# Kernel optimization log

Measured on AMD Instinct MI355X. Metric: run time of the kernel, lower is better.

Reference implementation:

```python
import jax, jax.numpy as jnp
import numpy as np

N, L, E, H = 8, 1024, 512, 4


def setup_inputs() -> dict:
    key = jax.random.key(0)
    ks = jax.random.split(key, 10)
    s = 1.0 / np.sqrt(E)
    return {
        "modalA": jax.random.normal(ks[0], (N, L, E), dtype=jnp.float32),
        "modalB": jax.random.normal(ks[1], (N, L, E), dtype=jnp.float32),
        "WqA": jax.random.normal(ks[2], (E, E), dtype=jnp.float32) * s,
        "bqA": jax.random.normal(ks[3], (E,), dtype=jnp.float32) * s,
        "WkA": jax.random.normal(ks[4], (E, E), dtype=jnp.float32) * s,
        "bkA": jax.random.normal(ks[5], (E,), dtype=jnp.float32) * s,
        "WqB": jax.random.normal(ks[6], (E, E), dtype=jnp.float32) * s,
        "bqB": jax.random.normal(ks[7], (E,), dtype=jnp.float32) * s,
        "WkB": jax.random.normal(ks[8], (E, E), dtype=jnp.float32) * s,
        "bkB": jax.random.normal(ks[9], (E,), dtype=jnp.float32) * s,
    }


def reference(modalA, modalB, WqA, bqA, WkA, bkA, WqB, bqB, WkB, bkB):
    # torch Linear: y = x @ W.T + b
    qA = modalA @ WqA.T + bqA  # [N, L, E]
    kA = modalA @ WkA.T + bkA
    qB = modalB @ WqB.T + bqB
    kB = modalB @ WkB.T + bkB

    # mean over heads of per-head dot products == full-dim dot / num_heads
    # (algebraically identical to einsum('nqhd,nkhd->nhqk').mean(1))
    inv_scale = 1.0 / (H * np.sqrt(E).astype(np.float32))

    def attn(q, k):
        scores = jnp.einsum('nqd,nkd->nqk', q, k) * inv_scale  # [N, L, L]
        return jax.nn.softmax(scores, axis=-1)

    weighted_A = attn(qA, kA)
    weighted_B = attn(qB, kB)
    weighted_AB = attn(qA, kB)
    weighted_BA = attn(qB, kA)

    cat_lower = jnp.concatenate([weighted_A, weighted_AB], axis=-1)  # [N, L, 2L]
    cat_upper = jnp.concatenate([weighted_B, weighted_BA], axis=-1)  # [N, L, 2L]
    cat = jnp.concatenate([cat_lower, cat_upper], axis=1)            # [N, 2L, 2L]
    return jnp.mean(cat, axis=0)                                     # [2L, 2L]
```

## Files before the change

kernel.cpp:

```cpp
#include <hip/hip_runtime.h>
#include <hip/hip_bf16.h>

typedef __bf16 bf16;
typedef bf16 bf16x8 __attribute__((ext_vector_type(8)));
typedef _Float16 f16;
typedef f16 f16x8 __attribute__((ext_vector_type(8)));
typedef float f32x4 __attribute__((ext_vector_type(4)));

constexpr int LL = 1024;
constexpr int EE = 512;
constexpr int NBATCH = 8;

__device__ __forceinline__ f32x4 mfma16(bf16x8 a, bf16x8 b, f32x4 c) {
    return __builtin_amdgcn_mfma_f32_16x16x32_bf16(a, b, c, 0, 0, 0);
}

#define GLOAD_LDS16(g, l)                                                     \
    __builtin_amdgcn_global_load_lds(                                         \
        (const __attribute__((address_space(1))) void*)(g),                   \
        (__attribute__((address_space(3))) void*)(l), 16, 0, 0)

__device__ __forceinline__ void wave_barrier() {
    __asm__ volatile("" ::: "memory");
    __builtin_amdgcn_s_barrier();
    __asm__ volatile("" ::: "memory");
}

constexpr int WAIT_VM6 = 0xF76;
constexpr int WAIT_VM0 = 0xF70;

struct CvtParams {
    const float* src[4];
    bf16* dst[4];
    int n8[4];
};

__global__ __launch_bounds__(256) void cvt_kernel(CvtParams p) {
    const int y = blockIdx.y;
    const float* __restrict__ src = p.src[y];
    bf16* __restrict__ dst = p.dst[y];
    const int n8 = p.n8[y];
    for (int i = blockIdx.x * 256 + threadIdx.x; i < n8; i += gridDim.x * 256) {
        float4 a = *(const float4*)(src + (size_t)i * 8);
        float4 b = *(const float4*)(src + (size_t)i * 8 + 4);
        bf16x8 o;
        o[0] = (bf16)a.x; o[1] = (bf16)a.y; o[2] = (bf16)a.z; o[3] = (bf16)a.w;
        o[4] = (bf16)b.x; o[5] = (bf16)b.y; o[6] = (bf16)b.z; o[7] = (bf16)b.w;
        *(bf16x8*)(dst + (size_t)i * 8) = o;
    }
}

struct ProjParams {
    const float* x[4];
    const bf16* w[4];
    const float* b[4];
};

__global__ __launch_bounds__(256, 2) void proj_kernel(ProjParams p, bf16* __restrict__ outbase) {
    const int f = blockIdx.x;
    const int xcd = f & 7;
    const int u = f >> 3;
    const int mz = xcd >> 2;
    const int by = (xcd & 3) * 16 + (u & 15);
    const int zq = (u >> 4) & 1;
    const int bxp = u >> 5;
    const int z = mz * 2 + zq;

    const float* __restrict__ X = p.x[z];
    const bf16* __restrict__ W = p.w[z];
    const float* __restrict__ Bv = p.b[z];
    bf16* __restrict__ O = outbase + (size_t)z * (NBATCH * LL) * EE;

    __shared__ union {
        struct {
            alignas(16) float Af[2][128][32];
            alignas(16) bf16  Bs[2][256][32];
        } st;
        alignas(16) bf16 ep[64][264];
    } sm;

    const int t = threadIdx.x;
    const int lane = t & 63, wid = t >> 6;
    const int wm = wid & 1, wn = wid >> 1;
    const int lr = lane & 15, kg = lane >> 4;

    f32x4 acc[4][8] = {};

    const int ar = t >> 3;
    const int ac = t & 7;
    const int sA = (ar >> 1) & 7;
    const int agc = (ac ^ sA) * 4;
    const float* Xrow0 = X + (size_t)(by * 128 + ar) * EE + agc;

    const int srow = t >> 2;
    const int cgl = t & 3;
    const int gcg = (cgl ^ ((srow >> 1) & 3)) * 8;
    const int scg = (kg ^ ((lr >> 1) & 3)) * 8;
    const bf16* Wrow0 = W + (size_t)(bxp * 256 + srow) * EE + gcg;

    const int cgLo = (2 * kg) ^ ((lr >> 1) & 7);
    const int cgHi = cgLo ^ 1;

    auto stage = [&](int k, int b) {
        const int k0 = k * 32;
#pragma unroll
        for (int i = 0; i < 4; ++i)
            GLOAD_LDS16(Xrow0 + (size_t)(32 * i) * EE + k0, &sm.st.Af[b][32 * i + ar][ac * 4]);
#pragma unroll
        for (int i = 0; i < 4; ++i)
            GLOAD_LDS16(Wrow0 + (size_t)(64 * i) * EE + k0, &sm.st.Bs[b][srow + 64 * i][cgl * 8]);
    };
    auto compute = [&](int b) {
        bf16x8 af[4], bfr[8];
#pragma unroll
        for (int im = 0; im < 4; ++im) {
            const int row = wm * 64 + im * 16 + lr;
            f32x4 lo = *(const f32x4*)&sm.st.Af[b][row][cgLo * 4];
            f32x4 hi = *(const f32x4*)&sm.st.Af[b][row][cgHi * 4];
#pragma unroll
            for (int e = 0; e < 4; ++e) {
                af[im][e] = (bf16)lo[e];
                af[im][4 + e] = (bf16)hi[e];
            }
        }
#pragma unroll
        for (int in = 0; in < 8; ++in)
            bfr[in] = *(const bf16x8*)&sm.st.Bs[b][wn * 128 + in * 16 + lr][scg];
#pragma unroll
        for (int im = 0; im < 4; ++im)
#pragma unroll
            for (int in = 0; in < 8; ++in)
                acc[im][in] = mfma16(af[im], bfr[in], acc[im][in]);
    };

    stage(0, 0);
#pragma unroll
    for (int k = 0; k < 16; ++k) {
        __builtin_amdgcn_s_waitcnt(WAIT_VM0);
        wave_barrier();
        if (k < 15) stage(k + 1, (k + 1) & 1);
        compute(k & 1);
    }
    __syncthreads();

#pragma unroll
    for (int pph = 0; pph < 2; ++pph) {
        if (wm == pph) {
#pragma unroll
            for (int im = 0; im < 4; ++im) {
                const int row = im * 16 + kg * 4;
#pragma unroll
                for (int in = 0; in < 8; ++in) {
                    const int col = wn * 128 + in * 16 + lr;
                    const float bias = Bv[bxp * 256 + col];
#pragma unroll
                    for (int r = 0; r < 4; ++r)
                        sm.ep[row + r][col] = (bf16)(acc[im][in][r] + bias);
                }
            }
        }
        __syncthreads();
#pragma unroll
        for (int i = 0; i < 8; ++i) {
            const int c = i * 256 + t;
            const int row = c >> 5, colg = (c & 31) * 8;
            *(uint4*)(O + (size_t)(by * 128 + pph * 64 + row) * EE + bxp * 256 + colg) =
                *(const uint4*)&sm.ep[row][colg];
        }
        __syncthreads();
    }
}

struct ScoresParams {
    const bf16* q[4];
    const bf16* k[4];
    f16* s[4];
};

__global__ __launch_bounds__(256, 2) void scores_kernel(ScoresParams p) {
    const int f = blockIdx.x;
    const int xcd = f & 7;
    const int j = f >> 3;
    const int z = (xcd << 2) + (j >> 5);
    const int map = z >> 3, n = z & 7;
    const int tile = j & 31;
    const int bxp = tile & 3, by = tile >> 2;

    const bf16* __restrict__ Qb = p.q[map] + (size_t)n * LL * EE;
    const bf16* __restrict__ Kb = p.k[map] + (size_t)n * LL * EE;
    f16* __restrict__ Sb = p.s[map] + (size_t)n * LL * LL;

    __shared__ union {
        struct { alignas(16) bf16 A[3][128][32]; alignas(16) bf16 B[3][256][32]; } st;
        alignas(16) f16 ep[64][264];
    } sm;

    const int t = threadIdx.x;
    const int lane = t & 63, wid = t >> 6;
    const int wm = wid & 1, wn = wid >> 1;
    const int lr = lane & 15, kg = lane >> 4;

    f32x4 acc[4][8] = {};

    const int srow = t >> 2;
    const int cgl = t & 3;
    const int gcg = (cgl ^ ((srow >> 1) & 3)) * 8;
    const int scg = (kg ^ ((lr >> 1) & 3)) * 8;

    const bf16* Qrow0 = Qb + (size_t)(by * 128 + srow) * EE + gcg;
    const bf16* Krow0 = Kb + (size_t)(bxp * 256 + srow) * EE + gcg;

    auto stage = [&](int k, int b) {
        const int k0 = k * 32;
#pragma unroll
        for (int i = 0; i < 2; ++i)
            GLOAD_LDS16(Qrow0 + (size_t)(64 * i) * EE + k0, &sm.st.A[b][srow + 64 * i][cgl * 8]);
#pragma unroll
        for (int i = 0; i < 4; ++i)
            GLOAD_LDS16(Krow0 + (size_t)(64 * i) * EE + k0, &sm.st.B[b][srow + 64 * i][cgl * 8]);
    };
    auto compute = [&](int b) {
        bf16x8 af[4], bfr[8];
#pragma unroll
        for (int im = 0; im < 4; ++im)
            af[im] = *(const bf16x8*)&sm.st.A[b][wm * 64 + im * 16 + lr][scg];
#pragma unroll
        for (int in = 0; in < 8; ++in)
            bfr[in] = *(const bf16x8*)&sm.st.B[b][wn * 128 + in * 16 + lr][scg];
#pragma unroll
        for (int im = 0; im < 4; ++im)
#pragma unroll
            for (int in = 0; in < 8; ++in)
                acc[im][in] = mfma16(af[im], bfr[in], acc[im][in]);
    };

    stage(0, 0);
    stage(1, 1);
#pragma unroll
    for (int k = 0; k < 16; ++k) {
        if (k < 15) __builtin_amdgcn_s_waitcnt(WAIT_VM6);
        else        __builtin_amdgcn_s_waitcnt(WAIT_VM0);
        wave_barrier();
        if (k < 14) stage(k + 2, (k + 2) % 3);
        compute(k % 3);
    }
    __syncthreads();

    const float inv_scale = 0.011048543456039806f;
#pragma unroll
    for (int pph = 0; pph < 2; ++pph) {
        if (wm == pph) {
#pragma unroll
            for (int im = 0; im < 4; ++im) {
                const int row = im * 16 + kg * 4;
#pragma unroll
                for (int in = 0; in < 8; ++in) {
                    const int col = wn * 128 + in * 16 + lr;
#pragma unroll
                    for (int r = 0; r < 4; ++r)
                        sm.ep[row + r][col] = (f16)(acc[im][in][r] * inv_scale);
                }
            }
        }
        __syncthreads();
#pragma unroll
        for (int i = 0; i < 8; ++i) {
            const int c = i * 256 + t;
            const int row = c >> 5, colg = (c & 31) * 8;
            *(uint4*)(Sb + (size_t)(by * 128 + pph * 64 + row) * LL + bxp * 256 + colg) =
                *(const uint4*)&sm.ep[row][colg];
        }
        __syncthreads();
    }
}

struct SmParams {
    const f16* s[4];
};

__global__ __launch_bounds__(256) void softmax_mean_kernel(SmParams p, float* __restrict__ out) {
    const int map = blockIdx.y;
    const f16* __restrict__ S = p.s[map];
    const int t = threadIdx.x;
    const int half = t >> 7;
    const int tl = t & 127;
    const int q = blockIdx.x * 2 + half;
    const int lane = t & 63, wid = t >> 6;
    __shared__ float red[NBATCH][4];

    f16x8 v[NBATCH];
#pragma unroll
    for (int n = 0; n < NBATCH; ++n)
        v[n] = *(const f16x8*)(S + ((size_t)n * LL + q) * LL + tl * 8);

    float e[NBATCH][8];
#pragma unroll
    for (int n = 0; n < NBATCH; ++n) {
        float s = 0.f;
#pragma unroll
        for (int j = 0; j < 8; ++j) {
            e[n][j] = __expf((float)v[n][j]);
            s += e[n][j];
        }
#pragma unroll
        for (int off = 32; off; off >>= 1) s += __shfl_xor(s, off);
        if (lane == 0) red[n][wid] = s;
    }
    __syncthreads();

    float acc[8] = {};
#pragma unroll
    for (int n = 0; n < NBATCH; ++n) {
        const float inv = 0.125f / (red[n][half * 2] + red[n][half * 2 + 1]);
#pragma unroll
        for (int j = 0; j < 8; ++j) acc[j] += e[n][j] * inv;
    }

    const int orow = (map >= 2 ? LL : 0) + q;
    const int ocol = (map & 1 ? LL : 0) + tl * 8;
    float* o = out + (size_t)orow * (2 * LL) + ocol;
    *(float4*)(o + 0) = make_float4(acc[0], acc[1], acc[2], acc[3]);
    *(float4*)(o + 4) = make_float4(acc[4], acc[5], acc[6], acc[7]);
}

extern "C" void kernel_launch(void* const* d_in, const int* in_sizes, int n_in,
                              void* d_out, int out_size, void* d_ws, size_t ws_size,
                              hipStream_t stream) {
    const float* modalA = (const float*)d_in[0];
    const float* modalB = (const float*)d_in[1];
    const float* WqA = (const float*)d_in[2];
    const float* bqA = (const float*)d_in[3];
    const float* WkA = (const float*)d_in[4];
    const float* bkA = (const float*)d_in[5];
    const float* WqB = (const float*)d_in[6];
    const float* bqB = (const float*)d_in[7];
    const float* WkB = (const float*)d_in[8];
    const float* bkB = (const float*)d_in[9];
    float* out = (float*)d_out;

    const size_t projN = (size_t)(NBATCH * LL) * EE;
    const size_t mapN = (size_t)NBATCH * LL * LL;
    char* base = (char*)d_ws;
    bf16* qk = (bf16*)base;
    char* region2 = base + 4 * projN * sizeof(bf16);
    bf16* W4 = (bf16*)region2;
    f16* S = (f16*)region2;

    CvtParams cp;
    const float* wsrc[4] = {WqA, WkA, WqB, WkB};
    for (int i = 0; i < 4; ++i) {
        cp.src[i] = wsrc[i];
        cp.dst[i] = W4 + (size_t)i * EE * EE;
        cp.n8[i] = EE * EE / 8;
    }
    cvt_kernel<<<dim3(128, 4), 256, 0, stream>>>(cp);

    ProjParams pp;
    pp.x[0] = modalA; pp.x[1] = modalA; pp.x[2] = modalB; pp.x[3] = modalB;
    for (int i = 0; i < 4; ++i) pp.w[i] = W4 + (size_t)i * EE * EE;
    pp.b[0] = bqA; pp.b[1] = bkA; pp.b[2] = bqB; pp.b[3] = bkB;
    proj_kernel<<<dim3(512), 256, 0, stream>>>(pp, qk);

    const bf16* qA = qk + 0 * projN;
    const bf16* kA = qk + 1 * projN;
    const bf16* qB = qk + 2 * projN;
    const bf16* kB = qk + 3 * projN;

    ScoresParams sp;
    sp.q[0] = qA; sp.q[1] = qA; sp.q[2] = qB; sp.q[3] = qB;
    sp.k[0] = kA; sp.k[1] = kB; sp.k[2] = kB; sp.k[3] = kA;
    for (int m = 0; m < 4; ++m) sp.s[m] = S + (size_t)m * mapN;
    scores_kernel<<<dim3(1024), 256, 0, stream>>>(sp);

    SmParams smp;
    for (int m = 0; m < 4; ++m) smp.s[m] = S + (size_t)m * mapN;
    softmax_mean_kernel<<<dim3(512, 4), 256, 0, stream>>>(smp, out);
}
```

Baseline: 170.9 us.

## Use 32x32x16 MFMA in score GEMM and relayout fp32 A tile in projection

Result: slower. 182.9 us (+7.0%).

```diff
diff --git a/kernel.cpp b/kernel.cpp
--- a/kernel.cpp
+++ b/kernel.cpp
@@ -6,6 +6,7 @@
 typedef _Float16 f16;
 typedef f16 f16x8 __attribute__((ext_vector_type(8)));
 typedef float f32x4 __attribute__((ext_vector_type(4)));
+typedef float f32x16 __attribute__((ext_vector_type(16)));
 
 constexpr int LL = 1024;
 constexpr int EE = 512;
@@ -13,6 +14,9 @@
 
 __device__ __forceinline__ f32x4 mfma16(bf16x8 a, bf16x8 b, f32x4 c) {
     return __builtin_amdgcn_mfma_f32_16x16x32_bf16(a, b, c, 0, 0, 0);
+}
+__device__ __forceinline__ f32x16 mfma32(bf16x8 a, bf16x8 b, f32x16 c) {
+    return __builtin_amdgcn_mfma_f32_32x32x16_bf16(a, b, c, 0, 0, 0);
 }
 
 #define GLOAD_LDS16(g, l)                                                     \
@@ -73,7 +77,7 @@
 
     __shared__ union {
         struct {
-            alignas(16) float Af[2][128][32];
+            alignas(16) float Af[2][4096];
             alignas(16) bf16  Bs[2][256][32];
         } st;
         alignas(16) bf16 ep[64][264];
@@ -86,11 +90,9 @@
 
     f32x4 acc[4][8] = {};
 
-    const int ar = t >> 3;
-    const int ac = t & 7;
-    const int sA = (ar >> 1) & 7;
-    const int agc = (ac ^ sA) * 4;
-    const float* Xrow0 = X + (size_t)(by * 128 + ar) * EE + agc;
+    const int kcT = (t >> 3) & 7;
+    const int ar0 = ((t >> 6) << 3) | (t & 7);
+    const float* Xst = X + (size_t)(by * 128 + ar0) * EE + kcT * 4;
 
     const int srow = t >> 2;
     const int cgl = t & 3;
@@ -98,14 +100,11 @@
     const int scg = (kg ^ ((lr >> 1) & 3)) * 8;
     const bf16* Wrow0 = W + (size_t)(bxp * 256 + srow) * EE + gcg;
 
-    const int cgLo = (2 * kg) ^ ((lr >> 1) & 7);
-    const int cgHi = cgLo ^ 1;
-
     auto stage = [&](int k, int b) {
         const int k0 = k * 32;
 #pragma unroll
         for (int i = 0; i < 4; ++i)
-            GLOAD_LDS16(Xrow0 + (size_t)(32 * i) * EE + k0, &sm.st.Af[b][32 * i + ar][ac * 4]);
+            GLOAD_LDS16(Xst + (size_t)(32 * i) * EE + k0, &sm.st.Af[b][(256 * i + t) * 4]);
 #pragma unroll
         for (int i = 0; i < 4; ++i)
             GLOAD_LDS16(Wrow0 + (size_t)(64 * i) * EE + k0, &sm.st.Bs[b][srow + 64 * i][cgl * 8]);
@@ -115,8 +114,9 @@
 #pragma unroll
         for (int im = 0; im < 4; ++im) {
             const int row = wm * 64 + im * 16 + lr;
-            f32x4 lo = *(const f32x4*)&sm.st.Af[b][row][cgLo * 4];
-            f32x4 hi = *(const f32x4*)&sm.st.Af[b][row][cgHi * 4];
+            const int sr = ((row >> 3) << 6) + (row & 7);
+            f32x4 lo = *(const f32x4*)&sm.st.Af[b][(sr + kg * 16) * 4];
+            f32x4 hi = *(const f32x4*)&sm.st.Af[b][(sr + kg * 16 + 8) * 4];
 #pragma unroll
             for (int e = 0; e < 4; ++e) {
                 af[im][e] = (bf16)lo[e];
@@ -198,14 +198,14 @@
     const int t = threadIdx.x;
     const int lane = t & 63, wid = t >> 6;
     const int wm = wid & 1, wn = wid >> 1;
-    const int lr = lane & 15, kg = lane >> 4;
-
-    f32x4 acc[4][8] = {};
+    const int arow = lane & 31;
+    const int kh = lane >> 5;
+
+    f32x16 acc[2][4] = {};
 
     const int srow = t >> 2;
     const int cgl = t & 3;
     const int gcg = (cgl ^ ((srow >> 1) & 3)) * 8;
-    const int scg = (kg ^ ((lr >> 1) & 3)) * 8;
 
     const bf16* Qrow0 = Qb + (size_t)(by * 128 + srow) * EE + gcg;
     const bf16* Krow0 = Kb + (size_t)(bxp * 256 + srow) * EE + gcg;
@@ -220,18 +220,34 @@
             GLOAD_LDS16(Krow0 + (size_t)(64 * i) * EE + k0, &sm.st.B[b][srow + 64 * i][cgl * 8]);
     };
     auto compute = [&](int b) {
-        bf16x8 af[4], bfr[8];
-#pragma unroll
-        for (int im = 0; im < 4; ++im)
-            af[im] = *(const bf16x8*)&sm.st.A[b][wm * 64 + im * 16 + lr][scg];
-#pragma unroll
-        for (int in = 0; in < 8; ++in)
-            bfr[in] = *(const bf16x8*)&sm.st.B[b][wn * 128 + in * 16 + lr][scg];
-#pragma unroll
-        for (int im = 0; im < 4; ++im)
-#pragma unroll
-            for (int in = 0; in < 8; ++in)
-                acc[im][in] = mfma16(af[im], bfr[in], acc[im][in]);
+        bf16x8 af[2][2], bfr[4][2];
+#pragma unroll
+        for (int im = 0; im < 2; ++im) {
+            const int row = wm * 64 + im * 32 + arow;
+            const int sw = (row >> 1) & 3;
+#pragma unroll
+            for (int jj = 0; jj < 2; ++jj) {
+                const int slot = (2 * jj + kh) ^ sw;
+                af[im][jj] = *(const bf16x8*)&sm.st.A[b][row][slot * 8];
+            }
+        }
+#pragma unroll
+        for (int in = 0; in < 4; ++in) {
+            const int row = wn * 128 + in * 32 + arow;
+            const int sw = (row >> 1) & 3;
+#pragma unroll
+            for (int jj = 0; jj < 2; ++jj) {
+                const int slot = (2 * jj + kh) ^ sw;
+                bfr[in][jj] = *(const bf16x8*)&sm.st.B[b][row][slot * 8];
+            }
+        }
+#pragma unroll
+        for (int im = 0; im < 2; ++im)
+#pragma unroll
+            for (int in = 0; in < 4; ++in)
+#pragma unroll
+                for (int jj = 0; jj < 2; ++jj)
+                    acc[im][in] = mfma32(af[im][jj], bfr[in][jj], acc[im][in]);
     };
 
     stage(0, 0);
@@ -251,16 +267,16 @@
     for (int pph = 0; pph < 2; ++pph) {
         if (wm == pph) {
 #pragma unroll
-            for (int im = 0; im < 4; ++im) {
-                const int row = im * 16 + kg * 4;
-#pragma unroll
-                for (int in = 0; in < 8; ++in) {
-                    const int col = wn * 128 + in * 16 + lr;
-#pragma unroll
-                    for (int r = 0; r < 4; ++r)
-                        sm.ep[row + r][col] = (f16)(acc[im][in][r] * inv_scale);
+            for (int im = 0; im < 2; ++im)
+#pragma unroll
+                for (int in = 0; in < 4; ++in) {
+                    const int col = wn * 128 + in * 32 + arow;
+#pragma unroll
+                    for (int reg = 0; reg < 16; ++reg) {
+                        const int rowl = im * 32 + (reg & 3) + 8 * (reg >> 2) + 4 * kh;
+                        sm.ep[rowl][col] = (f16)(acc[im][in][reg] * inv_scale);
+                    }
                 }
-            }
         }
         __syncthreads();
 #pragma unroll
```
